# Kernel tuning notes

Measured on AMD Instinct MI355X. Metric: run time of the kernel, lower is better.

The kernel has to match this reference:

```python
import jax, jax.numpy as jnp
import numpy as np

B, S, D, F, E, CAP = 4, 2048, 1024, 4096, 8, 320


def setup_inputs() -> dict:
    key = jax.random.key(0)
    k1, k2, k3, k4 = jax.random.split(key, 4)
    return {
        "hidden_states": jax.random.normal(k1, (B, S, D), dtype=jnp.float32),
        "router_w": jax.random.normal(k2, (D, E), dtype=jnp.float32) * 0.02,
        "wi": jax.random.normal(k3, (E, D, F), dtype=jnp.float32) * 0.02,
        "wo": jax.random.normal(k4, (E, F, D), dtype=jnp.float32) * 0.02,
    }


def reference(hidden_states, router_w, wi, wo):
    # ---- Router (Switch top-1 with per-sequence expert capacity) ----
    b, s, d = hidden_states.shape
    e = router_w.shape[1]
    logits = hidden_states.astype(jnp.float32) @ router_w          # [B,S,E]
    probs = jax.nn.softmax(logits, axis=-1)                        # [B,S,E]
    expert_idx = jnp.argmax(probs, axis=-1)                        # [B,S]
    onehot = jax.nn.one_hot(expert_idx, e, dtype=jnp.int32)        # [B,S,E]
    priority = jnp.cumsum(onehot, axis=1)                          # cumsum over seq dim (dim=-2)
    keep = onehot * (priority <= CAP).astype(jnp.int32)            # capacity-masked router_mask

    # slot of each token within its chosen expert (0-based)
    slot = jnp.take_along_axis(priority, expert_idx[..., None], axis=-1)[..., 0] - 1  # [B,S]
    valid = slot < CAP                                             # dropped tokens exceed capacity
    slot_sc = jnp.where(valid, slot, CAP)                          # out-of-range -> dropped by scatter

    b_ar = jnp.broadcast_to(jnp.arange(b)[:, None], (b, s))
    s_ar = jnp.broadcast_to(jnp.arange(s)[None, :], (b, s))
    dispatch = jnp.zeros((b, e, CAP), jnp.int32).at[b_ar, expert_idx, slot_sc].set(
        s_ar.astype(jnp.int32), mode="drop")                       # [B,E,CAP] token index per slot
    slot_used = jnp.zeros((b, e, CAP), bool).at[b_ar, expert_idx, slot_sc].set(
        valid, mode="drop")                                        # [B,E,CAP]

    # ---- Dispatch: gather tokens into [B,E,CAP,D] ----
    xg = jax.vmap(lambda xb, ib: xb[ib])(hidden_states, dispatch)  # [B,E,CAP,D]

    # ---- Per-expert dense FFN (grouped GEMM) ----
    hg = jax.nn.relu(jnp.einsum("becd,edf->becf", xg, wi))         # [B,E,CAP,F]
    yg = jnp.einsum("becf,efd->becd", hg, wo)                      # [B,E,CAP,D]

    # ---- Combine: scatter expert outputs back; unrouted tokens keep input ----
    idx_back = jnp.where(slot_used, dispatch, s)                   # out-of-range -> dropped
    next_states = jax.vmap(
        lambda xb, ib, yb: xb.at[ib.reshape(-1)].set(yb.reshape(-1, d), mode="drop")
    )(hidden_states, idx_back, yg)                                 # [B,S,D]

    max_prob = jnp.max(probs, axis=-1, keepdims=True)              # [B,S,1]
    out = max_prob * next_states
    expert_index_out = jnp.argmax(keep, axis=-1)                   # [B,S] (0 for dropped tokens)
    return out, logits, expert_index_out
```

## Files before the change

kernel.cpp:

```cpp
#include <hip/hip_runtime.h>
#include <hip/hip_bf16.h>
#include <stdint.h>

#define B_ 4
#define S_ 2048
#define D_ 1024
#define F_ 4096
#define E_ 8
#define CAP_ 320
#define BS_ (B_*S_)
#define MPE 1280

typedef unsigned short u16;
typedef __attribute__((ext_vector_type(8))) short bf16x8;
typedef __attribute__((ext_vector_type(4))) float f32x4;
typedef __attribute__((ext_vector_type(4))) unsigned short u16x4;
typedef __attribute__((ext_vector_type(8))) unsigned short u16x8;

__device__ __forceinline__ u16 f2bf(float f) {
  union { float f; uint32_t u; } v; v.f = f;
  uint32_t r = (v.u + 0x7FFFu + ((v.u >> 16) & 1u)) >> 16;
  return (u16)r;
}

__device__ __forceinline__ void gload16(const void* g, void* l) {
  __builtin_amdgcn_global_load_lds(
      (const __attribute__((address_space(1))) uint32_t*)g,
      (__attribute__((address_space(3))) uint32_t*)l, 16, 0, 0);
}

__device__ __forceinline__ void transpose_block(
    const float* __restrict__ W, u16* __restrict__ WT,
    const int K, const int N, const int bid, void* ldsraw)
{
  float (*tile)[65] = (float(*)[65])ldsraw;
  const int tk = K >> 7, tn = N >> 6;
  const int e = bid / (tk * tn), r = bid % (tk * tn);
  const int k0 = (r / tn) << 7, n0 = (r % tn) << 6;
  const float* We = W + (size_t)e * K * N;
  u16* WTe = WT + (size_t)e * N * K;
  const int t = threadIdx.x;
  const int fr = t >> 2, c0 = (t & 3) * 16;
#pragma unroll
  for (int j = 0; j < 4; ++j) {
    const float4 v = *(const float4*)(We + (size_t)(k0 + fr) * N + n0 + c0 + j * 4);
    tile[fr][c0 + j*4 + 0] = v.x; tile[fr][c0 + j*4 + 1] = v.y;
    tile[fr][c0 + j*4 + 2] = v.z; tile[fr][c0 + j*4 + 3] = v.w;
  }
  __syncthreads();
  const int nr = t >> 3, kk0 = (t & 7) * 16;
  u16x8 o0, o1;
#pragma unroll
  for (int j = 0; j < 8; ++j) o0[j] = f2bf(tile[kk0 + j][nr]);
#pragma unroll
  for (int j = 0; j < 8; ++j) o1[j] = f2bf(tile[kk0 + 8 + j][nr]);
  u16* dst = WTe + (size_t)(n0 + nr) * K + k0 + kk0;
  *(u16x8*)dst = o0;
  *(u16x8*)(dst + 8) = o1;
}

__global__ __launch_bounds__(512) void transpose_kernel(
    const float* __restrict__ W, u16* __restrict__ WT, const int K, const int N)
{
  __shared__ __align__(16) float tile[128][65];
  transpose_block(W, WT, K, N, blockIdx.x, (void*)tile);
}

__global__ __launch_bounds__(512) void prep_kernel(
    const float* __restrict__ hs, const float* __restrict__ rw,
    const float* __restrict__ wi, u16* __restrict__ wT,
    float* __restrict__ logits, float* __restrict__ maxp,
    int* __restrict__ eidx, const int twiT)
{
  __shared__ __align__(16) float tile[128][65];
  if ((int)blockIdx.x < twiT) {
    transpose_block(wi, wT, D_, F_, blockIdx.x, (void*)tile);
    return;
  }
  const int wv = threadIdx.x >> 6, l = threadIdx.x & 63;
  const int token = (blockIdx.x - twiT) * 8 + wv;
  const float* row = hs + (size_t)token * D_;
  const float4* rw4 = (const float4*)rw;

  double acc0=0, acc1=0, acc2=0, acc3=0, acc4=0, acc5=0, acc6=0, acc7=0;
#pragma unroll
  for (int j = 0; j < 4; ++j) {
    const int d4 = l + j * 64;
    const float4 v = ((const float4*)row)[d4];
#pragma unroll
    for (int c = 0; c < 4; ++c) {
      const int d = d4 * 4 + c;
      const float x = (&v.x)[c];
      const float4 w0 = rw4[d * 2];
      const float4 w1 = rw4[d * 2 + 1];
      acc0 += (double)x * (double)w0.x;
      acc1 += (double)x * (double)w0.y;
      acc2 += (double)x * (double)w0.z;
      acc3 += (double)x * (double)w0.w;
      acc4 += (double)x * (double)w1.x;
      acc5 += (double)x * (double)w1.y;
      acc6 += (double)x * (double)w1.z;
      acc7 += (double)x * (double)w1.w;
    }
  }
  double acc[E_] = {acc0, acc1, acc2, acc3, acc4, acc5, acc6, acc7};
#pragma unroll
  for (int e = 0; e < E_; ++e) {
#pragma unroll
    for (int off = 32; off; off >>= 1)
      acc[e] += __shfl_xor(acc[e], off);
  }
  if (l == 0) {
    float lg[E_];
#pragma unroll
    for (int e = 0; e < E_; ++e) lg[e] = (float)acc[e];
    float lmax = lg[0]; int am = 0;
#pragma unroll
    for (int e = 1; e < E_; ++e) { if (lg[e] > lmax) { lmax = lg[e]; am = e; } }
    float sum = 0.f;
#pragma unroll
    for (int e = 0; e < E_; ++e) sum += expf(lg[e] - lmax);
#pragma unroll
    for (int e = 0; e < E_; ++e) logits[(size_t)token * E_ + e] = lg[e];
    maxp[token] = 1.0f / sum;
    eidx[token] = am;
  }
}

__global__ __launch_bounds__(256) void scan_kernel(
    const int* __restrict__ eidx, int* __restrict__ tok,
    float* __restrict__ eout, const float* __restrict__ hs,
    const float* __restrict__ maxp, float* __restrict__ out)
{
  const int b = blockIdx.x >> 3, e = blockIdx.x & 7;
  __shared__ int wsum[4];
  const int tid = threadIdx.x, wv = tid >> 6, l = tid & 63;
  for (int i = tid; i < CAP_; i += 256) tok[(b * E_ + e) * CAP_ + i] = -1;
  __syncthreads();
  int base = 0;
  for (int ch = 0; ch < S_ / 256; ++ch) {
    const int s = ch * 256 + tid;
    const bool p = (eidx[b * S_ + s] == e);
    const unsigned long long m = __ballot(p);
    const int lp = __popcll(m & ((1ULL << l) - 1ULL));
    if (l == 0) wsum[wv] = __popcll(m);
    __syncthreads();
    int pre = 0, tot = 0;
#pragma unroll
    for (int w = 0; w < 4; ++w) { if (w < wv) pre += wsum[w]; tot += wsum[w]; }
    if (p) {
      const int rank = base + pre + lp;
      if (rank < CAP_) {
        tok[(b * E_ + e) * CAP_ + rank] = s;
        eout[b * S_ + s] = (float)e;
      } else {
        eout[b * S_ + s] = 0.0f;
        const float mp = maxp[b * S_ + s];
        const float4* src = (const float4*)(hs + (size_t)(b * S_ + s) * D_);
        float4* dst = (float4*)(out + (size_t)(b * S_ + s) * D_);
        for (int j = 0; j < D_ / 4; ++j) {
          const float4 vv = src[j];
          float4 o; o.x = vv.x * mp; o.y = vv.y * mp; o.z = vv.z * mp; o.w = vv.w * mp;
          dst[j] = o;
        }
      }
    }
    base += tot;
    __syncthreads();
  }
}

__global__ __launch_bounds__(256) void gather_kernel(
    const float* __restrict__ hs, const int* __restrict__ tok,
    u16* __restrict__ Xg)
{
  const int bx = blockIdx.x;
  const int e = bx / MPE, r = bx % MPE;
  const int b = r / CAP_, c = r % CAP_;
  const int t = tok[(b * E_ + e) * CAP_ + c];
  const int d = threadIdx.x * 4;
  u16x4 o;
  if (t >= 0) {
    const float4 vv = *(const float4*)(hs + ((size_t)(b * S_ + t)) * D_ + d);
    o[0] = f2bf(vv.x); o[1] = f2bf(vv.y); o[2] = f2bf(vv.z); o[3] = f2bf(vv.w);
  } else {
    o[0] = 0; o[1] = 0; o[2] = 0; o[3] = 0;
  }
  *(u16x4*)(Xg + (size_t)bx * D_ + d) = o;
}

#define BAR() __builtin_amdgcn_s_barrier()
#define LGKM0() do { asm volatile("s_waitcnt lgkmcnt(0)" ::: "memory");    \
                     __builtin_amdgcn_sched_barrier(0); } while (0)
#define VMW(n) asm volatile("s_waitcnt vmcnt(" #n ")" ::: "memory")

__global__ __launch_bounds__(512, 2) void moe_g1(
    const u16* __restrict__ Aall, const u16* __restrict__ Btall,
    u16* __restrict__ hgout, const int gemm_blocks,
    const float* __restrict__ Wtr, u16* __restrict__ WTtr)
{
  __shared__ __align__(16) u16 lds[49152];

#define LDA(p, h) (lds + (p) * 8192 + (h) * 4096)
#define LDB(p, h) (lds + 16384 + (p) * 16384 + (h) * 8192)

  if ((int)blockIdx.x >= gemm_blocks) {
    transpose_block(Wtr, WTtr, F_, D_, blockIdx.x - gemm_blocks, (void*)lds);
    return;
  }
  const int K = D_, NT = K >> 6, N = F_;
  const int cpx = gemm_blocks >> 3;
  const int bid = blockIdx.x;
  const int swzb = (bid & 7) * cpx + (bid >> 3);
  const int e = swzb / 160, rem = swzb % 160;
  const int m0 = (rem / 16) * 128, n0 = (rem % 16) * 256;

  const u16* Ae = Aall + (size_t)e * MPE * K;
  const u16* Be = Btall + (size_t)e * N * K;

  const int tid = threadIdx.x;
  const int wv = tid >> 6, l = tid & 63;
  const int wr = wv >> 2, wc = wv & 3;
  const int lr = l & 15, lk = l >> 4;
  const int rswz = ((lr >> 3) & 1) << 4;
  const int gs0 = tid ^ (((tid >> 5) & 1) << 1);
  const size_t goffB = (size_t)((gs0 >> 2) & 127) * K + (size_t)((gs0 & 3) * 8);
  const size_t goffA = (size_t)((gs0 >> 2) & 63) * K
                     + (size_t)(((gs0 >> 8) & 1) * 32) + (size_t)((gs0 & 3) * 8);
  const int dwoff = wv * 512;

  const u16* pA0 = Ae + (size_t)m0 * K;
  const u16* pA1 = Ae + (size_t)(m0 + 64) * K;
  const u16* pB0 = Be + (size_t)n0 * K;
  const u16* pB1 = Be + (size_t)(n0 + 128) * K;

  f32x4 acc[4][4];
#pragma unroll
  for (int i = 0; i < 4; ++i)
#pragma unroll
    for (int j = 0; j < 4; ++j) acc[i][j] = (f32x4){0.f, 0.f, 0.f, 0.f};

  bf16x8 fa[4], fb0[4], fb1[4];

#define STAGE_A(dhalf, rb, tt) \
    gload16((rb) + goffA + (size_t)((tt) * 64), (dhalf) + dwoff)

#define STAGE_B(dhalf, rb, tt) do {                                        \
    const u16* s_ = (rb) + goffB + (size_t)((tt) * 64);                    \
    gload16(s_,      (dhalf) + dwoff);                                     \
    gload16(s_ + 32, (dhalf) + 4096 + dwoff);                              \
  } while (0)

#define READ_A1(msub, p) do {                                              \
    _Pragma("unroll")                                                      \
    for (int mf = 0; mf < 2; ++mf)                                         \
      _Pragma("unroll")                                                    \
      for (int kk = 0; kk < 2; ++kk)                                       \
        fa[mf*2+kk] = *(const bf16x8*)&LDA(p, wr)                          \
            [(kk*64 + ((msub)*2+mf)*16 + lr)*32 + ((lk*8) ^ rswz)];        \
  } while (0)

#define READ_B1(nsub, p, fb) do {                                          \
    _Pragma("unroll")                                                      \
    for (int nf = 0; nf < 2; ++nf)                                         \
      _Pragma("unroll")                                                    \
      for (int kk = 0; kk < 2; ++kk)                                       \
        fb[nf*2+kk] = *(const bf16x8*)&LDB(p, wc>>1)                       \
            [(kk*128 + (wc&1)*64 + (nsub)*32 + nf*16 + lr)*32              \
             + ((lk*8) ^ rswz)];                                           \
  } while (0)

#define MFMA1(msub, nsub, fb) do {                                        \
    __builtin_amdgcn_s_setprio(1);                                         \
    _Pragma("unroll")                                                      \
    for (int mf = 0; mf < 2; ++mf)                                         \
      _Pragma("unroll")                                                    \
      for (int nf = 0; nf < 2; ++nf)                                       \
        _Pragma("unroll")                                                  \
        for (int kk = 0; kk < 2; ++kk)                                     \
          acc[(msub)*2+mf][(nsub)*2+nf] =                                  \
              __builtin_amdgcn_mfma_f32_16x16x32_bf16(                     \
                  fa[mf*2+kk], fb[nf*2+kk],                                \
                  acc[(msub)*2+mf][(nsub)*2+nf], 0, 0, 0);                 \
    __builtin_amdgcn_s_setprio(0);                                         \
  } while (0)

#define DO_TILE1(p, pn, tc) do {                                           \
                                                                   \
    READ_A1(0, p); READ_B1(0, p, fb0);                                     \
    if ((tc) + 1 < NT) STAGE_A(LDA(pn, 1), pA1, (tc) + 1);                 \
    BAR(); LGKM0();                                                        \
    MFMA1(0, 0, fb0);                                                      \
    BAR();                                                                 \
                                                                   \
    READ_B1(1, p, fb1);                                                    \
    BAR(); LGKM0();                                                        \
    MFMA1(0, 1, fb1);                                                      \
    BAR();                                                                 \
                                                                   \
    READ_A1(1, p);                                                         \
    if ((tc) + 2 < NT) STAGE_B(LDB(p, 0), pB0, (tc) + 2);                  \
    BAR(); LGKM0();                                                        \
    MFMA1(1, 0, fb0);                                                      \
    BAR();                                                                 \
                                                                   \
    if ((tc) + 2 < NT) {                                                   \
      STAGE_B(LDB(p, 1), pB1, (tc) + 2);                                   \
      STAGE_A(LDA(p, 0), pA0, (tc) + 2);                                   \
    }                                                                      \
    BAR();                                                                 \
    MFMA1(1, 1, fb1);                                                      \
    if ((tc) >= NT - 2) VMW(0); else VMW(5);                               \
    BAR();                                                                 \
  } while (0)

  STAGE_A(LDA(0, 0), pA0, 0);
  STAGE_A(LDA(0, 1), pA1, 0);
  STAGE_B(LDB(0, 0), pB0, 0);
  STAGE_B(LDB(0, 1), pB1, 0);
  STAGE_B(LDB(1, 0), pB0, 1);
  STAGE_B(LDB(1, 1), pB1, 1);
  STAGE_A(LDA(1, 0), pA0, 1);
  VMW(5); BAR();

  for (int t = 0; t < NT; t += 2) {
    DO_TILE1(0, 1, t);
    DO_TILE1(1, 0, t + 1);
  }

#pragma unroll
  for (int i = 0; i < 4; ++i) {
#pragma unroll
    for (int r = 0; r < 4; ++r) {
      const int grow = m0 + wr * 64 + i * 16 + lk * 4 + r;
      u16* hrow = hgout + ((size_t)e * MPE + grow) * (size_t)N + n0 + wc * 64;
#pragma unroll
      for (int j = 0; j < 4; ++j)
        hrow[j * 16 + lr] = f2bf(fmaxf(acc[i][j][r], 0.0f));
    }
  }
#undef LDA
#undef LDB
#undef STAGE_A
#undef STAGE_B
#undef READ_A1
#undef READ_B1
#undef MFMA1
#undef DO_TILE1
}

__global__ __launch_bounds__(512, 2) void moe_g2(
    const u16* __restrict__ Aall, const u16* __restrict__ Btall,
    float* __restrict__ out, const int* __restrict__ tok,
    const float* __restrict__ maxp)
{
  __shared__ __align__(16) u16 lds[2][2][2][8192];

  const int K = F_, NT = K >> 6, N = D_;
  const int gemm_blocks = 160, cpx = gemm_blocks >> 3;
  const int bid = blockIdx.x;
  const int swzb = (bid & 7) * cpx + (bid >> 3);
  const int e = swzb / 20, rem = swzb % 20;
  const int m0 = (rem / 4) * 256, n0 = (rem % 4) * 256;

  const u16* Ae = Aall + (size_t)e * MPE * K;
  const u16* Be = Btall + (size_t)e * N * K;

  const int tid = threadIdx.x;
  const int wv = tid >> 6, l = tid & 63;
  const int wr = wv >> 2, wc = wv & 3;
  const int lr = l & 15, lk = l >> 4;
  const int rswz = ((lr >> 3) & 1) << 4;
  const int gs0 = tid ^ (((tid >> 5) & 1) << 1);
  const size_t goff = (size_t)((gs0 >> 2) & 127) * K + (size_t)((gs0 & 3) * 8);
  const int dwoff = wv * 512;

  const u16* pA0 = Ae + (size_t)m0 * K;
  const u16* pA1 = Ae + (size_t)(m0 + 128) * K;
  const u16* pB0 = Be + (size_t)n0 * K;
  const u16* pB1 = Be + (size_t)(n0 + 128) * K;

  f32x4 acc[8][4];
#pragma unroll
  for (int i = 0; i < 8; ++i)
#pragma unroll
    for (int j = 0; j < 4; ++j) acc[i][j] = (f32x4){0.f, 0.f, 0.f, 0.f};

  bf16x8 fa[8], fb0[4], fb1[4];

#define LDSH(p, ab, h) (&lds[p][ab][h][0])

#define STAGE(dhalf, rb, tt) do {                                          \
    const u16* s_ = (rb) + goff + (size_t)((tt) * 64);                     \
    gload16(s_,      (dhalf) + dwoff);                                     \
    gload16(s_ + 32, (dhalf) + 4096 + dwoff);                              \
  } while (0)

#define READ_A(msub, p) do {                                               \
    _Pragma("unroll")                                                      \
    for (int mf = 0; mf < 4; ++mf)                                         \
      _Pragma("unroll")                                                    \
      for (int kk = 0; kk < 2; ++kk)                                       \
        fa[mf*2+kk] = *(const bf16x8*)&lds[p][0][wr]                       \
            [(kk*128 + (msub)*64 + mf*16 + lr)*32 + ((lk*8) ^ rswz)];      \
  } while (0)

#define READ_B(nsub, p, fb) do {                                           \
    _Pragma("unroll")                                                      \
    for (int nf = 0; nf < 2; ++nf)                                         \
      _Pragma("unroll")                                                    \
      for (int kk = 0; kk < 2; ++kk)                                       \
        fb[nf*2+kk] = *(const bf16x8*)&lds[p][1][wc>>1]                    \
            [(kk*128 + (wc&1)*64 + (nsub)*32 + nf*16 + lr)*32              \
             + ((lk*8) ^ rswz)];                                           \
  } while (0)

#define MFMA_Q(msub, nsub, fb) do {                                        \
    __builtin_amdgcn_s_setprio(1);                                         \
    _Pragma("unroll")                                                      \
    for (int mf = 0; mf < 4; ++mf)                                         \
      _Pragma("unroll")                                                    \
      for (int nf = 0; nf < 2; ++nf)                                       \
        _Pragma("unroll")                                                  \
        for (int kk = 0; kk < 2; ++kk)                                     \
          acc[(msub)*4+mf][(nsub)*2+nf] =                                  \
              __builtin_amdgcn_mfma_f32_16x16x32_bf16(                     \
                  fa[mf*2+kk], fb[nf*2+kk],                                \
                  acc[(msub)*4+mf][(nsub)*2+nf], 0, 0, 0);                 \
    __builtin_amdgcn_s_setprio(0);                                         \
  } while (0)

#define DO_TILE(p, pn, tc) do {                                            \
    READ_A(0, p); READ_B(0, p, fb0);                                       \
    if ((tc) + 1 < NT) STAGE(LDSH(pn, 0, 1), pA1, (tc) + 1);               \
    BAR(); LGKM0();                                                        \
    MFMA_Q(0, 0, fb0);                                                     \
    BAR();                                                                 \
    READ_B(1, p, fb1);                                                     \
    BAR(); LGKM0();                                                        \
    MFMA_Q(0, 1, fb1);                                                     \
    BAR();                                                                 \
    READ_A(1, p);                                                          \
    if ((tc) + 2 < NT) STAGE(LDSH(p, 1, 0), pB0, (tc) + 2);                \
    BAR(); LGKM0();                                                        \
    MFMA_Q(1, 0, fb0);                                                     \
    BAR();                                                                 \
    if ((tc) + 2 < NT) {                                                   \
      STAGE(LDSH(p, 1, 1), pB1, (tc) + 2);                                 \
      STAGE(LDSH(p, 0, 0), pA0, (tc) + 2);                                 \
    }                                                                      \
    BAR();                                                                 \
    MFMA_Q(1, 1, fb1);                                                     \
    if ((tc) >= NT - 2) VMW(0); else VMW(6);                               \
    BAR();                                                                 \
  } while (0)

  STAGE(LDSH(0, 0, 0), pA0, 0);
  STAGE(LDSH(0, 0, 1), pA1, 0);
  STAGE(LDSH(0, 1, 0), pB0, 0);
  STAGE(LDSH(0, 1, 1), pB1, 0);
  STAGE(LDSH(1, 0, 0), pA0, 1);
  STAGE(LDSH(1, 1, 0), pB0, 1);
  STAGE(LDSH(1, 1, 1), pB1, 1);
  VMW(6); BAR();

  for (int t = 0; t < NT; t += 2) {
    DO_TILE(0, 1, t);
    DO_TILE(1, 0, t + 1);
  }

#pragma unroll
  for (int i = 0; i < 8; ++i) {
#pragma unroll
    for (int r = 0; r < 4; ++r) {
      const int grow = m0 + wr * 128 + i * 16 + lk * 4 + r;
      const int b = grow / CAP_, c = grow % CAP_;
      const int t = tok[(b * E_ + e) * CAP_ + c];
      if (t >= 0) {
        const float sc = maxp[b * S_ + t];
        float* orow = out + ((size_t)(b * S_ + t)) * D_ + n0 + wc * 64;
#pragma unroll
        for (int j = 0; j < 4; ++j)
          orow[j * 16 + lr] = sc * acc[i][j][r];
      }
    }
  }
#undef LDSH
#undef STAGE
#undef READ_A
#undef READ_B
#undef MFMA_Q
#undef DO_TILE
}

extern "C" void kernel_launch(void* const* d_in, const int* in_sizes, int n_in,
                              void* d_out, int out_size, void* d_ws, size_t ws_size,
                              hipStream_t stream)
{
  const float* hs = (const float*)d_in[0];
  const float* rw = (const float*)d_in[1];
  const float* wi = (const float*)d_in[2];
  const float* wo = (const float*)d_in[3];

  float* out    = (float*)d_out;
  float* logits = out + (size_t)BS_ * D_;
  float* eout   = logits + (size_t)BS_ * E_;

  uint8_t* ws = (uint8_t*)d_ws;
  int*   tok  = (int*)(ws + 0);
  float* maxp = (float*)(ws + 40960);
  int*   eidx = (int*)(ws + 73728);
  u16*   Xg   = (u16*)(ws + 131072);
  u16*   hg   = (u16*)(ws + 21102592);
  u16*   wiT  = (u16*)(ws + 104988672);
  if (ws_size < 172097536ULL) return;
  const bool big = ws_size >= 239206400ULL;
  u16* woT = big ? (u16*)(ws + 172097536) : wiT;

  const int twiT = E_ * (D_ / 128) * (F_ / 64);
  const int twoT = E_ * (F_ / 128) * (D_ / 64);
  const int g1 = E_ * (MPE / 128) * (F_ / 256);
  const int g2 = 160;

  prep_kernel<<<twiT + BS_ / 8, 512, 0, stream>>>(
      hs, rw, wi, wiT, logits, maxp, eidx, twiT);
  scan_kernel<<<B_ * E_, 256, 0, stream>>>(eidx, tok, eout, hs, maxp, out);
  gather_kernel<<<E_ * MPE, 256, 0, stream>>>(hs, tok, Xg);

  if (big) {
    moe_g1<<<g1 + twoT, 512, 0, stream>>>(Xg, wiT, hg, g1, wo, woT);
  } else {
    moe_g1<<<g1, 512, 0, stream>>>(Xg, wiT, hg, g1, nullptr, nullptr);
    transpose_kernel<<<twoT, 512, 0, stream>>>(wo, woT, F_, D_);
  }
  moe_g2<<<g2, 512, 0, stream>>>(hg, woT, out, tok, maxp);
}
```

Before: 345.3 us.

## Software-pipeline LDS fragment reads against MFMAs with partial lgkmcnt waits in both GEMMs

```diff
diff --git a/kernel.cpp b/kernel.cpp
--- a/kernel.cpp
+++ b/kernel.cpp
@@ -190,8 +190,8 @@
 }
 
 #define BAR() __builtin_amdgcn_s_barrier()
-#define LGKM0() do { asm volatile("s_waitcnt lgkmcnt(0)" ::: "memory");    \
-                     __builtin_amdgcn_sched_barrier(0); } while (0)
+#define LGKMN(n) do { asm volatile("s_waitcnt lgkmcnt(" #n ")" ::: "memory"); \
+                      __builtin_amdgcn_sched_barrier(0); } while (0)
 #define VMW(n) asm volatile("s_waitcnt vmcnt(" #n ")" ::: "memory")
 
 __global__ __launch_bounds__(512, 2) void moe_g1(
@@ -240,92 +240,75 @@
 #pragma unroll
     for (int j = 0; j < 4; ++j) acc[i][j] = (f32x4){0.f, 0.f, 0.f, 0.f};
 
-  bf16x8 fa[4], fb0[4], fb1[4];
-
-#define STAGE_A(dhalf, rb, tt) \
+  bf16x8 faA[2], faB[2], fb[8];
+
+#define STAGE_A1(dhalf, rb, tt) \
     gload16((rb) + goffA + (size_t)((tt) * 64), (dhalf) + dwoff)
 
-#define STAGE_B(dhalf, rb, tt) do {                                        \
+#define STAGE_B1(dhalf, rb, tt) do {                                       \
     const u16* s_ = (rb) + goffB + (size_t)((tt) * 64);                    \
     gload16(s_,      (dhalf) + dwoff);                                     \
     gload16(s_ + 32, (dhalf) + 4096 + dwoff);                              \
   } while (0)
 
-#define READ_A1(msub, p) do {                                              \
+#define READ_AQ1(q, p, fa_) do {                                           \
     _Pragma("unroll")                                                      \
-    for (int mf = 0; mf < 2; ++mf)                                         \
-      _Pragma("unroll")                                                    \
-      for (int kk = 0; kk < 2; ++kk)                                       \
-        fa[mf*2+kk] = *(const bf16x8*)&LDA(p, wr)                          \
-            [(kk*64 + ((msub)*2+mf)*16 + lr)*32 + ((lk*8) ^ rswz)];        \
-  } while (0)
-
-#define READ_B1(nsub, p, fb) do {                                          \
+    for (int kk = 0; kk < 2; ++kk)                                         \
+      fa_[kk] = *(const bf16x8*)&LDA(p, wr)                                \
+          [(kk*64 + (q)*16 + lr)*32 + ((lk*8) ^ rswz)];                    \
+  } while (0)
+
+#define READ_B_ALL1(p) do {                                                \
     _Pragma("unroll")                                                      \
-    for (int nf = 0; nf < 2; ++nf)                                         \
+    for (int nf = 0; nf < 4; ++nf)                                         \
       _Pragma("unroll")                                                    \
       for (int kk = 0; kk < 2; ++kk)                                       \
         fb[nf*2+kk] = *(const bf16x8*)&LDB(p, wc>>1)                       \
-            [(kk*128 + (wc&1)*64 + (nsub)*32 + nf*16 + lr)*32              \
+            [(kk*128 + (wc&1)*64 + (nf>>1)*32 + (nf&1)*16 + lr)*32         \
              + ((lk*8) ^ rswz)];                                           \
   } while (0)
 
-#define MFMA1(msub, nsub, fb) do {                                        \
+#define MFMA_P1(q, fa_) do {                                               \
     __builtin_amdgcn_s_setprio(1);                                         \
     _Pragma("unroll")                                                      \
-    for (int mf = 0; mf < 2; ++mf)                                         \
+    for (int nf = 0; nf < 4; ++nf)                                         \
       _Pragma("unroll")                                                    \
-      for (int nf = 0; nf < 2; ++nf)                                       \
-        _Pragma("unroll")                                                  \
-        for (int kk = 0; kk < 2; ++kk)                                     \
-          acc[(msub)*2+mf][(nsub)*2+nf] =                                  \
-              __builtin_amdgcn_mfma_f32_16x16x32_bf16(                     \
-                  fa[mf*2+kk], fb[nf*2+kk],                                \
-                  acc[(msub)*2+mf][(nsub)*2+nf], 0, 0, 0);                 \
+      for (int kk = 0; kk < 2; ++kk)                                       \
+        acc[q][nf] = __builtin_amdgcn_mfma_f32_16x16x32_bf16(              \
+            fa_[kk], fb[nf*2+kk], acc[q][nf], 0, 0, 0);                    \
     __builtin_amdgcn_s_setprio(0);                                         \
   } while (0)
 
-#define DO_TILE1(p, pn, tc) do {                                           \
-                                                                   \
-    READ_A1(0, p); READ_B1(0, p, fb0);                                     \
-    if ((tc) + 1 < NT) STAGE_A(LDA(pn, 1), pA1, (tc) + 1);                 \
-    BAR(); LGKM0();                                                        \
-    MFMA1(0, 0, fb0);                                                      \
+#define DO_T1(p, pn, tc) do {                                              \
+    READ_AQ1(1, p, faB);                                                   \
+    if ((tc) + 1 < NT) { STAGE_A1(LDA(pn,0), pA0, (tc)+1);                 \
+                         STAGE_A1(LDA(pn,1), pA1, (tc)+1); }               \
+    LGKMN(2); MFMA_P1(0, faA);                                             \
+    READ_AQ1(2, p, faA);                                                   \
+    LGKMN(2); MFMA_P1(1, faB);                                             \
     BAR();                                                                 \
-                                                                   \
-    READ_B1(1, p, fb1);                                                    \
-    BAR(); LGKM0();                                                        \
-    MFMA1(0, 1, fb1);                                                      \
+    READ_AQ1(3, p, faB);                                                   \
+    if ((tc) + 2 < NT) { STAGE_B1(LDB(p,0), pB0, (tc)+2);                  \
+                         STAGE_B1(LDB(p,1), pB1, (tc)+2); }                \
+    LGKMN(2); MFMA_P1(2, faA);                                             \
+    LGKMN(0); MFMA_P1(3, faB);                                             \
+    if ((tc) >= NT - 2) VMW(0); else VMW(4);                               \
     BAR();                                                                 \
-                                                                   \
-    READ_A1(1, p);                                                         \
-    if ((tc) + 2 < NT) STAGE_B(LDB(p, 0), pB0, (tc) + 2);                  \
-    BAR(); LGKM0();                                                        \
-    MFMA1(1, 0, fb0);                                                      \
-    BAR();                                                                 \
-                                                                   \
-    if ((tc) + 2 < NT) {                                                   \
-      STAGE_B(LDB(p, 1), pB1, (tc) + 2);                                   \
-      STAGE_A(LDA(p, 0), pA0, (tc) + 2);                                   \
-    }                                                                      \
-    BAR();                                                                 \
-    MFMA1(1, 1, fb1);                                                      \
-    if ((tc) >= NT - 2) VMW(0); else VMW(5);                               \
-    BAR();                                                                 \
-  } while (0)
-
-  STAGE_A(LDA(0, 0), pA0, 0);
-  STAGE_A(LDA(0, 1), pA1, 0);
-  STAGE_B(LDB(0, 0), pB0, 0);
-  STAGE_B(LDB(0, 1), pB1, 0);
-  STAGE_B(LDB(1, 0), pB0, 1);
-  STAGE_B(LDB(1, 1), pB1, 1);
-  STAGE_A(LDA(1, 0), pA0, 1);
-  VMW(5); BAR();
+    if ((tc) + 1 < NT) { READ_B_ALL1(pn); READ_AQ1(0, pn, faA); }          \
+  } while (0)
+
+  STAGE_A1(LDA(0,0), pA0, 0);
+  STAGE_A1(LDA(0,1), pA1, 0);
+  STAGE_B1(LDB(0,0), pB0, 0);
+  STAGE_B1(LDB(0,1), pB1, 0);
+  STAGE_B1(LDB(1,0), pB0, 1);
+  STAGE_B1(LDB(1,1), pB1, 1);
+  VMW(4); BAR();
+  READ_B_ALL1(0); READ_AQ1(0, 0, faA);
 
   for (int t = 0; t < NT; t += 2) {
-    DO_TILE1(0, 1, t);
-    DO_TILE1(1, 0, t + 1);
+    DO_T1(0, 1, t);
+    DO_T1(1, 0, t + 1);
   }
 
 #pragma unroll
@@ -341,12 +324,12 @@
   }
 #undef LDA
 #undef LDB
-#undef STAGE_A
-#undef STAGE_B
-#undef READ_A1
-#undef READ_B1
-#undef MFMA1
-#undef DO_TILE1
+#undef STAGE_A1
+#undef STAGE_B1
+#undef READ_AQ1
+#undef READ_B_ALL1
+#undef MFMA_P1
+#undef DO_T1
 }
 
 __global__ __launch_bounds__(512, 2) void moe_g2(
@@ -386,87 +369,78 @@
 #pragma unroll
     for (int j = 0; j < 4; ++j) acc[i][j] = (f32x4){0.f, 0.f, 0.f, 0.f};
 
-  bf16x8 fa[8], fb0[4], fb1[4];
+  bf16x8 faA[4], faB[4], fb[8];
 
 #define LDSH(p, ab, h) (&lds[p][ab][h][0])
 
-#define STAGE(dhalf, rb, tt) do {                                          \
+#define STAGE2(dhalf, rb, tt) do {                                         \
     const u16* s_ = (rb) + goff + (size_t)((tt) * 64);                     \
     gload16(s_,      (dhalf) + dwoff);                                     \
     gload16(s_ + 32, (dhalf) + 4096 + dwoff);                              \
   } while (0)
 
-#define READ_A(msub, p) do {                                               \
+#define READ_AQ2(q, p, fa_) do {                                           \
     _Pragma("unroll")                                                      \
-    for (int mf = 0; mf < 4; ++mf)                                         \
+    for (int mf = 0; mf < 2; ++mf)                                         \
       _Pragma("unroll")                                                    \
       for (int kk = 0; kk < 2; ++kk)                                       \
-        fa[mf*2+kk] = *(const bf16x8*)&lds[p][0][wr]                       \
-            [(kk*128 + (msub)*64 + mf*16 + lr)*32 + ((lk*8) ^ rswz)];      \
-  } while (0)
-
-#define READ_B(nsub, p, fb) do {                                           \
+        fa_[mf*2+kk] = *(const bf16x8*)&lds[p][0][wr]                      \
+            [(kk*128 + (q)*32 + mf*16 + lr)*32 + ((lk*8) ^ rswz)];         \
+  } while (0)
+
+#define READ_B_ALL2(p) do {                                                \
     _Pragma("unroll")                                                      \
-    for (int nf = 0; nf < 2; ++nf)                                         \
+    for (int nf = 0; nf < 4; ++nf)                                         \
       _Pragma("unroll")                                                    \
       for (int kk = 0; kk < 2; ++kk)                                       \
         fb[nf*2+kk] = *(const bf16x8*)&lds[p][1][wc>>1]                    \
-            [(kk*128 + (wc&1)*64 + (nsub)*32 + nf*16 + lr)*32              \
+            [(kk*128 + (wc&1)*64 + (nf>>1)*32 + (nf&1)*16 + lr)*32         \
              + ((lk*8) ^ rswz)];                                           \
   } while (0)
 
-#define MFMA_Q(msub, nsub, fb) do {                                        \
+#define MFMA_P2(q, fa_) do {                                               \
     __builtin_amdgcn_s_setprio(1);                                         \
     _Pragma("unroll")                                                      \
-    for (int mf = 0; mf < 4; ++mf)                                         \
+    for (int mf = 0; mf < 2; ++mf)                                         \
       _Pragma("unroll")                                                    \
-      for (int nf = 0; nf < 2; ++nf)                                       \
+      for (int nf = 0; nf < 4; ++nf)                                       \
         _Pragma("unroll")                                                  \
         for (int kk = 0; kk < 2; ++kk)                                     \
-          acc[(msub)*4+mf][(nsub)*2+nf] =                                  \
-              __builtin_amdgcn_mfma_f32_16x16x32_bf16(                     \
-                  fa[mf*2+kk], fb[nf*2+kk],                                \
-                  acc[(msub)*4+mf][(nsub)*2+nf], 0, 0, 0);                 \
+          acc[(q)*2+mf][nf] = __builtin_amdgcn_mfma_f32_16x16x32_bf16(     \
+              fa_[mf*2+kk], fb[nf*2+kk], acc[(q)*2+mf][nf], 0, 0, 0);      \
     __builtin_amdgcn_s_setprio(0);                                         \
   } while (0)
 
-#define DO_TILE(p, pn, tc) do {                                            \
-    READ_A(0, p); READ_B(0, p, fb0);                                       \
-    if ((tc) + 1 < NT) STAGE(LDSH(pn, 0, 1), pA1, (tc) + 1);               \
-    BAR(); LGKM0();                                                        \
-    MFMA_Q(0, 0, fb0);                                                     \
+#define DO_T2(p, pn, tc) do {                                              \
+    READ_AQ2(1, p, faB);                                                   \
+    if ((tc) + 1 < NT) { STAGE2(LDSH(pn,0,0), pA0, (tc)+1);                \
+                         STAGE2(LDSH(pn,0,1), pA1, (tc)+1); }              \
+    LGKMN(4); MFMA_P2(0, faA);                                             \
+    READ_AQ2(2, p, faA);                                                   \
+    LGKMN(4); MFMA_P2(1, faB);                                             \
     BAR();                                                                 \
-    READ_B(1, p, fb1);                                                     \
-    BAR(); LGKM0();                                                        \
-    MFMA_Q(0, 1, fb1);                                                     \
+    READ_AQ2(3, p, faB);                                                   \
+    if ((tc) + 2 < NT) { STAGE2(LDSH(p,1,0), pB0, (tc)+2);                 \
+                         STAGE2(LDSH(p,1,1), pB1, (tc)+2); }               \
+    LGKMN(4); MFMA_P2(2, faA);                                             \
+    LGKMN(0); MFMA_P2(3, faB);                                             \
+    if ((tc) >= NT - 2) VMW(0); else VMW(4);                               \
     BAR();                                                                 \
-    READ_A(1, p);                                                          \
-    if ((tc) + 2 < NT) STAGE(LDSH(p, 1, 0), pB0, (tc) + 2);                \
-    BAR(); LGKM0();                                                        \
-    MFMA_Q(1, 0, fb0);                                                     \
-    BAR();                                                                 \
-    if ((tc) + 2 < NT) {                                                   \
-      STAGE(LDSH(p, 1, 1), pB1, (tc) + 2);                                 \
-      STAGE(LDSH(p, 0, 0), pA0, (tc) + 2);                                 \
-    }                                                                      \
-    BAR();                                                                 \
-    MFMA_Q(1, 1, fb1);                                                     \
-    if ((tc) >= NT - 2) VMW(0); else VMW(6);                               \
-    BAR();                                                                 \
-  } while (0)
-
-  STAGE(LDSH(0, 0, 0), pA0, 0);
-  STAGE(LDSH(0, 0, 1), pA1, 0);
-  STAGE(LDSH(0, 1, 0), pB0, 0);
-  STAGE(LDSH(0, 1, 1), pB1, 0);
-  STAGE(LDSH(1, 0, 0), pA0, 1);
-  STAGE(LDSH(1, 1, 0), pB0, 1);
-  STAGE(LDSH(1, 1, 1), pB1, 1);
-  VMW(6); BAR();
+    if ((tc) + 1 < NT) { READ_B_ALL2(pn); READ_AQ2(0, pn, faA); }          \
+  } while (0)
+
+  STAGE2(LDSH(0,0,0), pA0, 0);
+  STAGE2(LDSH(0,0,1), pA1, 0);
+  STAGE2(LDSH(0,1,0), pB0, 0);
+  STAGE2(LDSH(0,1,1), pB1, 0);
+  STAGE2(LDSH(1,1,0), pB0, 1);
+  STAGE2(LDSH(1,1,1), pB1, 1);
+  VMW(4); BAR();
+  READ_B_ALL2(0); READ_AQ2(0, 0, faA);
 
   for (int t = 0; t < NT; t += 2) {
-    DO_TILE(0, 1, t);
-    DO_TILE(1, 0, t + 1);
+    DO_T2(0, 1, t);
+    DO_T2(1, 0, t + 1);
   }
 
 #pragma unroll
@@ -486,11 +460,11 @@
     }
   }
 #undef LDSH
-#undef STAGE
-#undef READ_A
-#undef READ_B
-#undef MFMA_Q
-#undef DO_TILE
+#undef STAGE2
+#undef READ_AQ2
+#undef READ_B_ALL2
+#undef MFMA_P2
+#undef DO_T2
 }
 
 extern "C" void kernel_launch(void* const* d_in, const int* in_sizes, int n_in,
```

Result: faster. 330.6 us (-4.3%).
